# Performance work log

Measured on AMD Instinct MI355X. Metric: run time of the kernel, lower is better.

The kernel has to match this reference:

```python
import jax, jax.numpy as jnp
import numpy as np

N_NODES = 50000
N_EDGES = 600000
NUM_RELS = 5
IN_CH = 768
HID = 128
OUT_CH = 128
REL_DIM = 200


def _segment_softmax(scores, seg, n):
    # numerically stable softmax over variable-size segments (destination nodes)
    m = jax.ops.segment_max(scores, seg, num_segments=n)
    e = jnp.exp(scores - m[seg])
    s = jax.ops.segment_sum(e, seg, num_segments=n)
    return e / s[seg]


def _hgn_conv(x, edge_index, edge_type, W, Wr, a, Wres, rel_tab, final):
    # x: [N, h_in]; W: [h, h_in]; Wr: [h, rel_dim]; a: [3h]; rel_tab: [R, rel_dim]
    src = edge_index[0]
    dst = edge_index[1]
    n = x.shape[0]
    h = W.shape[0]
    Wx = x @ W.T                      # [N, h] (shared by x_i, x_j, messages)
    rel = rel_tab[edge_type] @ Wr.T   # [E, h]
    aA, aB, aC = a[:h], a[h:2 * h], a[2 * h:]
    # a([Wx_i | Wx_j | Wr rel]) decomposed to avoid materializing the concat
    score = Wx[dst] @ aA + Wx[src] @ aB + rel @ aC   # [E]
    alpha = jax.nn.leaky_relu(score, 0.2)
    alpha = _segment_softmax(alpha, dst, n)
    agg = jax.ops.segment_sum(Wx[src] * alpha[:, None], dst, num_segments=n)
    out = jax.nn.elu(agg + x @ Wres.T)
    if final:
        out = out / jnp.maximum(jnp.linalg.norm(out, axis=1, keepdims=True), 1e-12)
    return out, alpha


def setup_inputs() -> dict:
    key = jax.random.key(0)
    ks = jax.random.split(key, 20)
    s = 0.02
    return {
        "x": jax.random.normal(ks[0], (N_NODES, IN_CH), jnp.float32),
        "edge_index": jax.random.randint(ks[1], (2, N_EDGES), 0, N_NODES, jnp.int64 if jax.config.jax_enable_x64 else jnp.int32),
        "edge_type": jax.random.randint(ks[2], (N_EDGES,), 0, NUM_RELS, jnp.int64 if jax.config.jax_enable_x64 else jnp.int32),
        "l1_W": jax.random.normal(ks[3], (HID, IN_CH), jnp.float32) * s,
        "l1_b": jnp.zeros((HID,), jnp.float32),
        "l2_W": jax.random.normal(ks[4], (OUT_CH, HID), jnp.float32) * s,
        "l2_b": jnp.zeros((OUT_CH,), jnp.float32),
        "W1": jax.random.normal(ks[5], (HID, HID), jnp.float32) * s,
        "Wr1": jax.random.normal(ks[6], (HID, REL_DIM), jnp.float32) * s,
        "a1": jax.random.normal(ks[7], (3 * HID,), jnp.float32) * s,
        "Wres1": jax.random.normal(ks[8], (HID, HID), jnp.float32) * s,
        "rel1": jax.random.normal(ks[9], (NUM_RELS, REL_DIM), jnp.float32),
        "W2": jax.random.normal(ks[10], (HID, HID), jnp.float32) * s,
        "Wr2": jax.random.normal(ks[11], (HID, REL_DIM), jnp.float32) * s,
        "a2": jax.random.normal(ks[12], (3 * HID,), jnp.float32) * s,
        "Wres2": jax.random.normal(ks[13], (HID, HID), jnp.float32) * s,
        "rel2": jax.random.normal(ks[14], (NUM_RELS, REL_DIM), jnp.float32),
    }


def reference(x, edge_index, edge_type, l1_W, l1_b, l2_W, l2_b,
              W1, Wr1, a1, Wres1, rel1, W2, Wr2, a2, Wres2, rel2):
    out = jax.nn.leaky_relu(x @ l1_W.T + l1_b, 0.01)
    # layer 1 (dropout is identity in eval mode)
    out, alpha = _hgn_conv(out, edge_index, edge_type, W1, Wr1, a1, Wres1, rel1, final=False)
    # layer 2: original code blends alpha into self.alpha but weights messages
    # with its own (unblended) softmax alpha, so pre_alpha does not affect output
    out, _ = _hgn_conv(out, edge_index, edge_type, W2, Wr2, a2, Wres2, rel2, final=True)
    out = jax.nn.leaky_relu(out @ l2_W.T + l2_b, 0.01)
    return out
```

## Files before the change

kernel.cpp:

```cpp
#include <hip/hip_runtime.h>

namespace {

typedef unsigned short ushort_t;
typedef unsigned int uint_t;
typedef __attribute__((ext_vector_type(8))) short bf16x8;
typedef __attribute__((ext_vector_type(4))) float f32x4;

constexpr int N   = 50000;
constexpr int E   = 600000;
constexpr int NR  = 5;
constexpr int KIN = 768;
constexpr int H   = 128;
constexpr int RD  = 200;

__device__ inline ushort_t f2b(float f){
  uint_t u = __builtin_bit_cast(uint_t, f);
  uint_t r = (u + 0x7FFFu + ((u >> 16) & 1u)) >> 16;
  return (ushort_t)r;
}
__device__ inline float b2f_lo(uint_t u){ return __builtin_bit_cast(float, u << 16); }
__device__ inline float b2f_hi(uint_t u){ return __builtin_bit_cast(float, u & 0xFFFF0000u); }
__device__ inline float b2f_us(ushort_t h){ return __builtin_bit_cast(float, ((uint_t)h) << 16); }

__global__ void prep_k(const float* __restrict__ l1W, const float* __restrict__ W1,
                       const float* __restrict__ R1, const float* __restrict__ W2,
                       const float* __restrict__ R2, const float* __restrict__ l2W,
                       ushort_t* __restrict__ wts, int* __restrict__ deg,
                       const float* __restrict__ rel1, const float* __restrict__ Wr1,
                       const float* __restrict__ a1, float* __restrict__ sC1,
                       const float* __restrict__ rel2, const float* __restrict__ Wr2,
                       const float* __restrict__ a2, float* __restrict__ sC2){
  constexpr int S0 = H * KIN;
  constexpr int S1 = H * H;
  int b = blockIdx.x, tid = threadIdx.x;
  if (b < 704){
    int i = b * 256 + tid;
    float v;
    if (i < S0) v = l1W[i];
    else {
      int j = i - S0, seg = j >> 14, off = j & (S1 - 1);
      const float* srcs[5] = {W1, R1, W2, R2, l2W};
      v = srcs[seg][off];
    }
    wts[i] = f2b(v);
  } else if (b < 900){
    int i = (b - 704) * 256 + tid;
    if (i < N) deg[i] = 0;
  } else {
    int L = b - 900;
    const float* rel = L ? rel2 : rel1;
    const float* Wr  = L ? Wr2  : Wr1;
    const float* a   = L ? a2   : a1;
    float*       sC  = L ? sC2  : sC1;
    __shared__ float red[256];
    int n = tid >> 1, half = tid & 1;
    float aC = a[256 + n];
    for (int r = 0; r < NR; ++r){
      float p = 0.f;
      for (int k = half * 100; k < half * 100 + 100; ++k)
        p += rel[r * RD + k] * Wr[n * RD + k];
      red[tid] = p * aC;
      __syncthreads();
      for (int s = 128; s > 0; s >>= 1){
        if (tid < s) red[tid] += red[tid + s];
        __syncthreads();
      }
      if (tid == 0) sC[r] = red[0];
      __syncthreads();
    }
  }
}

__global__ void degcount_k(const int* __restrict__ dst, int* __restrict__ deg){
  int e = blockIdx.x * 256 + threadIdx.x;
  if (e < E) atomicAdd(&deg[dst[e]], 1);
}

__global__ void scan1_k(const int* __restrict__ deg, int* __restrict__ chunk,
                        int* __restrict__ bsums, int n){
  __shared__ int s[256];
  int tid = threadIdx.x, i = blockIdx.x * 256 + tid;
  int v = (i < n) ? deg[i] : 0;
  s[tid] = v; __syncthreads();
  for (int off = 1; off < 256; off <<= 1){
    int t = (tid >= off) ? s[tid - off] : 0;
    __syncthreads();
    s[tid] += t;
    __syncthreads();
  }
  if (i < n) chunk[i] = s[tid] - v;
  if (tid == 255) bsums[blockIdx.x] = s[255];
}

__global__ void scan2_k(const int* __restrict__ bsums, int* __restrict__ boffs, int nb){
  __shared__ int s[256];
  int tid = threadIdx.x;
  int v = (tid < nb) ? bsums[tid] : 0;
  s[tid] = v; __syncthreads();
  for (int off = 1; off < 256; off <<= 1){
    int t = (tid >= off) ? s[tid - off] : 0;
    __syncthreads();
    s[tid] += t;
    __syncthreads();
  }
  if (tid < nb) boffs[tid] = s[tid] - v;
}

__global__ void scan3_k(int* __restrict__ rowptr, const int* __restrict__ boffs,
                        int* __restrict__ cursor, int n, int total){
  int i = blockIdx.x * 256 + threadIdx.x;
  if (i < n){
    int v = rowptr[i] + boffs[blockIdx.x];
    rowptr[i] = v; cursor[i] = v;
  }
  if (i == 0) rowptr[n] = total;
}

__global__ void fill_k(const int* __restrict__ src, const int* __restrict__ dst,
                       const int* __restrict__ et, int* __restrict__ cursor,
                       int* __restrict__ cpk){
  int e = blockIdx.x * 256 + threadIdx.x;
  if (e < E){
    int d = dst[e];
    int p = atomicAdd(&cursor[d], 1);
    cpk[p] = src[e] | (et[e] << 16);
  }
}

template<int K1, int M1, bool AFP32, bool NORM, bool STORE1, int M2>
__global__ __launch_bounds__(256) void gfused_k(
    const void* __restrict__ Ap, const ushort_t* __restrict__ Wb1,
    const float* __restrict__ bias1, const ushort_t* __restrict__ aggM,
    ushort_t* __restrict__ out1,
    const ushort_t* __restrict__ Wb2, const float* __restrict__ vec2,
    void* __restrict__ out2, float* __restrict__ sA, float* __restrict__ sB, int M)
{
  constexpr int AP = 40;
  constexpr int BP = 40;
  constexpr int CP = 136;
  __shared__ __align__(16) ushort_t As[64 * AP];
  __shared__ __align__(16) ushort_t Bs[128 * BP];
  __shared__ __align__(16) ushort_t Cs[64 * CP];
  const int tid  = threadIdx.x;
  const int wave = tid >> 6, lane = tid & 63;
  const int l15  = lane & 15, quad = lane >> 4;
  const int row0 = blockIdx.x * 64;

  if (M1 == 2){
    #pragma unroll
    for (int i = 0; i < 4; ++i){
      int idx = tid + 256 * i;
      int r = idx >> 4, c8 = idx & 15;
      int grow = row0 + r;
      uint4 v = make_uint4(0, 0, 0, 0);
      if (grow < M) v = *reinterpret_cast<const uint4*>(aggM + (size_t)grow * 128 + c8 * 8);
      *reinterpret_cast<uint4*>(&Cs[r * CP + c8 * 8]) = v;
    }
  }

  f32x4 acc[8];
  #pragma unroll
  for (int t = 0; t < 8; ++t) acc[t] = (f32x4){0.f, 0.f, 0.f, 0.f};

  for (int k0 = 0; k0 < K1; k0 += 32){
    {
      int r = tid >> 2, q = tid & 3;
      int grow = row0 + r;
      ushort_t v[8] = {0,0,0,0,0,0,0,0};
      if (grow < M){
        if (AFP32){
          const float* ap = (const float*)Ap + (size_t)grow * K1 + k0 + q * 8;
          float4 u0 = *reinterpret_cast<const float4*>(ap);
          float4 u1 = *reinterpret_cast<const float4*>(ap + 4);
          v[0]=f2b(u0.x); v[1]=f2b(u0.y); v[2]=f2b(u0.z); v[3]=f2b(u0.w);
          v[4]=f2b(u1.x); v[5]=f2b(u1.y); v[6]=f2b(u1.z); v[7]=f2b(u1.w);
        } else {
          const uint4 u = *reinterpret_cast<const uint4*>(
              (const ushort_t*)Ap + (size_t)grow * K1 + k0 + q * 8);
          *reinterpret_cast<uint4*>(v) = u;
        }
      }
      *reinterpret_cast<uint4*>(&As[r * AP + q * 8]) = *reinterpret_cast<uint4*>(v);
    }
    {
      int n = tid >> 1, seg = tid & 1;
      const ushort_t* wp = Wb1 + (size_t)n * K1 + k0 + seg * 16;
      uint4 v0 = *reinterpret_cast<const uint4*>(wp);
      uint4 v1 = *reinterpret_cast<const uint4*>(wp + 8);
      *reinterpret_cast<uint4*>(&Bs[n * BP + seg * 16])     = v0;
      *reinterpret_cast<uint4*>(&Bs[n * BP + seg * 16 + 8]) = v1;
    }
    __syncthreads();
    bf16x8 af = *reinterpret_cast<const bf16x8*>(&As[(wave * 16 + l15) * AP + quad * 8]);
    #pragma unroll
    for (int t = 0; t < 8; ++t){
      bf16x8 bfr = *reinterpret_cast<const bf16x8*>(&Bs[(t * 16 + l15) * BP + quad * 8]);
      acc[t] = __builtin_amdgcn_mfma_f32_16x16x32_bf16(af, bfr, acc[t], 0, 0, 0);
    }
    __syncthreads();
  }

  float vv[8][4];
  #pragma unroll
  for (int t = 0; t < 8; ++t){
    #pragma unroll
    for (int r = 0; r < 4; ++r){
      int lr  = wave * 16 + quad * 4 + r;
      int col = t * 16 + l15;
      float v = acc[t][r];
      if (M1 == 1){
        v += bias1[col];
        v = v > 0.f ? v : 0.01f * v;
      } else {
        v += b2f_us(Cs[lr * CP + col]);
        v = v > 0.f ? v : __expf(v) - 1.f;
      }
      vv[t][r] = v;
    }
  }
  if (NORM){
    #pragma unroll
    for (int r = 0; r < 4; ++r){
      float ss = 0.f;
      #pragma unroll
      for (int t = 0; t < 8; ++t) ss += vv[t][r] * vv[t][r];
      #pragma unroll
      for (int off = 1; off < 16; off <<= 1) ss += __shfl_xor(ss, off, 64);
      float sc = 1.f / fmaxf(sqrtf(ss), 1e-12f);
      #pragma unroll
      for (int t = 0; t < 8; ++t) vv[t][r] *= sc;
    }
  }
  #pragma unroll
  for (int t = 0; t < 8; ++t){
    #pragma unroll
    for (int r = 0; r < 4; ++r){
      int lr  = wave * 16 + quad * 4 + r;
      int col = t * 16 + l15;
      int grow = row0 + lr;
      ushort_t h = f2b(vv[t][r]);
      if (STORE1 && grow < M) out1[(size_t)grow * 128 + col] = h;
      Cs[lr * CP + col] = h;
    }
  }
  __syncthreads();

  #pragma unroll
  for (int t = 0; t < 8; ++t) acc[t] = (f32x4){0.f, 0.f, 0.f, 0.f};
  for (int k0 = 0; k0 < 128; k0 += 32){
    {
      int n = tid >> 1, seg = tid & 1;
      const ushort_t* wp = Wb2 + (size_t)n * 128 + k0 + seg * 16;
      uint4 v0 = *reinterpret_cast<const uint4*>(wp);
      uint4 v1 = *reinterpret_cast<const uint4*>(wp + 8);
      *reinterpret_cast<uint4*>(&Bs[n * BP + seg * 16])     = v0;
      *reinterpret_cast<uint4*>(&Bs[n * BP + seg * 16 + 8]) = v1;
    }
    __syncthreads();
    bf16x8 af = *reinterpret_cast<const bf16x8*>(&Cs[(wave * 16 + l15) * CP + k0 + quad * 8]);
    #pragma unroll
    for (int t = 0; t < 8; ++t){
      bf16x8 bfr = *reinterpret_cast<const bf16x8*>(&Bs[(t * 16 + l15) * BP + quad * 8]);
      acc[t] = __builtin_amdgcn_mfma_f32_16x16x32_bf16(af, bfr, acc[t], 0, 0, 0);
    }
    __syncthreads();
  }

  if (M2 == 1){
    #pragma unroll
    for (int t = 0; t < 8; ++t){
      #pragma unroll
      for (int r = 0; r < 4; ++r){
        int grow = row0 + wave * 16 + quad * 4 + r;
        if (grow >= M) continue;
        int col = t * 16 + l15;
        float v = acc[t][r] + vec2[col];
        v = v > 0.f ? v : 0.01f * v;
        ((float*)out2)[(size_t)grow * 128 + col] = v;
      }
    }
  } else {
    #pragma unroll
    for (int t = 0; t < 8; ++t){
      #pragma unroll
      for (int r = 0; r < 4; ++r){
        int grow = row0 + wave * 16 + quad * 4 + r;
        if (grow >= M) continue;
        int col = t * 16 + l15;
        ((ushort_t*)out2)[(size_t)grow * 128 + col] = f2b(acc[t][r]);
      }
    }
    #pragma unroll
    for (int r = 0; r < 4; ++r){
      float pa = 0.f, pb = 0.f;
      #pragma unroll
      for (int t = 0; t < 8; ++t){
        int col = t * 16 + l15;
        pa += acc[t][r] * vec2[col];
        pb += acc[t][r] * vec2[128 + col];
      }
      #pragma unroll
      for (int off = 1; off < 16; off <<= 1){
        pa += __shfl_xor(pa, off, 64);
        pb += __shfl_xor(pb, off, 64);
      }
      int grow = row0 + wave * 16 + quad * 4 + r;
      if (l15 == r && grow < M){ sA[grow] = pa; sB[grow] = pb; }
    }
  }
}

__global__ void agg_k(const ushort_t* __restrict__ Wx, const float* __restrict__ sA,
                      const float* __restrict__ sB, const float* __restrict__ sC,
                      const int* __restrict__ rowptr, const int* __restrict__ cpk,
                      uint_t* __restrict__ aggU, int n){
  int node = blockIdx.x * 4 + (threadIdx.x >> 6);
  int lane = threadIdx.x & 63;
  if (node >= n) return;
  int p0 = rowptr[node], p1 = rowptr[node + 1];
  int deg = p1 - p0;
  float sa = sA[node];
  float m = -1e30f, ssum = 0.f, a0 = 0.f, a1 = 0.f;

  for (int c0 = 0; c0 < deg; c0 += 64){
    int cnt = deg - c0; if (cnt > 64) cnt = 64;
    bool ok = lane < cnt;
    int p  = p0 + c0 + (ok ? lane : 0);
    int pk = cpk[p];
    int sn = pk & 0xFFFF;
    float s = sa + sB[sn] + sC[pk >> 16];
    s = s > 0.f ? s : 0.2f * s;
    float sv = ok ? s : -1e30f;
    #pragma unroll
    for (int off = 32; off > 0; off >>= 1) sv = fmaxf(sv, __shfl_xor(sv, off, 64));
    float mn = fmaxf(m, sv);
    float corr = __expf(m - mn);
    ssum *= corr; a0 *= corr; a1 *= corr;
    float ev = ok ? __expf(s - mn) : 0.f;
    float es = ev;
    #pragma unroll
    for (int off = 32; off > 0; off >>= 1) es += __shfl_xor(es, off, 64);
    ssum += es;
    int png = ok ? pk : 0;
    m = mn;

    for (int e = 0; e < cnt; e += 4){
      int  n0 = __shfl(png, e,     64) & 0xFFFF, n1 = __shfl(png, e + 1, 64) & 0xFFFF;
      int  n2 = __shfl(png, e + 2, 64) & 0xFFFF, n3 = __shfl(png, e + 3, 64) & 0xFFFF;
      float e0 = __shfl(ev, e,     64), e1 = __shfl(ev, e + 1, 64);
      float e2 = __shfl(ev, e + 2, 64), e3 = __shfl(ev, e + 3, 64);
      uint_t u0 = *reinterpret_cast<const uint_t*>(Wx + (size_t)n0 * 128 + lane * 2);
      uint_t u1 = *reinterpret_cast<const uint_t*>(Wx + (size_t)n1 * 128 + lane * 2);
      uint_t u2 = *reinterpret_cast<const uint_t*>(Wx + (size_t)n2 * 128 + lane * 2);
      uint_t u3 = *reinterpret_cast<const uint_t*>(Wx + (size_t)n3 * 128 + lane * 2);
      a0 += e0 * b2f_lo(u0); a1 += e0 * b2f_hi(u0);
      a0 += e1 * b2f_lo(u1); a1 += e1 * b2f_hi(u1);
      a0 += e2 * b2f_lo(u2); a1 += e2 * b2f_hi(u2);
      a0 += e3 * b2f_lo(u3); a1 += e3 * b2f_hi(u3);
    }
  }
  float inv = (deg > 0) ? 1.f / ssum : 0.f;
  uint_t o = (uint_t)f2b(a0 * inv) | ((uint_t)f2b(a1 * inv) << 16);
  aggU[(size_t)node * 64 + lane] = o;
}

}

extern "C" void kernel_launch(void* const* d_in, const int* in_sizes, int n_in,
                              void* d_out, int out_size, void* d_ws, size_t ws_size,
                              hipStream_t stream)
{
  const float* x     = (const float*)d_in[0];
  const int*   eidx  = (const int*)d_in[1];
  const int*   et    = (const int*)d_in[2];
  const float* l1W   = (const float*)d_in[3];
  const float* l1b   = (const float*)d_in[4];
  const float* l2W   = (const float*)d_in[5];
  const float* l2b   = (const float*)d_in[6];
  const float* W1    = (const float*)d_in[7];
  const float* Wr1   = (const float*)d_in[8];
  const float* a1    = (const float*)d_in[9];
  const float* Wres1 = (const float*)d_in[10];
  const float* rel1  = (const float*)d_in[11];
  const float* W2    = (const float*)d_in[12];
  const float* Wr2   = (const float*)d_in[13];
  const float* a2    = (const float*)d_in[14];
  const float* Wres2 = (const float*)d_in[15];
  const float* rel2  = (const float*)d_in[16];
  float* outp = (float*)d_out;

  const int* esrc = eidx;
  const int* edst = eidx + E;

  float* f = (float*)d_ws;
  size_t o = 0;
  float* sA   = f + o; o += N;
  float* sB   = f + o; o += N;
  float* sC1  = f + o; o += 8;
  float* sC2  = f + o; o += 8;
  ushort_t* us = (ushort_t*)(f + o);
  size_t ou = 0;
  ushort_t* b0   = us + ou; ou += (size_t)N * H;
  ushort_t* b1   = us + ou; ou += (size_t)N * H;
  ushort_t* Wxb  = us + ou; ou += (size_t)N * H;
  ushort_t* aggB = us + ou; ou += (size_t)N * H;
  ushort_t* wtsb = us + ou; ou += (size_t)H * KIN + 5 * H * H;
  ushort_t* l1Wb = wtsb;
  ushort_t* W1b  = wtsb + H * KIN;
  ushort_t* R1b  = W1b + H * H;
  ushort_t* W2b  = R1b + H * H;
  ushort_t* R2b  = W2b + H * H;
  ushort_t* l2Wb = R2b + H * H;
  if (ou & 1) ou += 1;
  int* wi = (int*)(us + ou);
  size_t oi = 0;
  int* deg    = wi + oi; oi += N;
  int* rowptr = wi + oi; oi += N + 1;
  int* cursor = wi + oi; oi += N;
  int* bsums  = wi + oi; oi += 256;
  int* boffs  = wi + oi; oi += 256;
  int* cpk    = wi + oi; oi += E;

  const int EB    = (E + 255) / 256;
  const int NB256 = (N + 255) / 256;
  const int GB    = (N + 63) / 64;
  const int NB4   = (N + 3) / 4;

  prep_k<<<902, 256, 0, stream>>>(l1W, W1, Wres1, W2, Wres2, l2W, wtsb, deg,
                                  rel1, Wr1, a1, sC1, rel2, Wr2, a2, sC2);
  degcount_k<<<EB, 256, 0, stream>>>(edst, deg);
  scan1_k<<<NB256, 256, 0, stream>>>(deg, rowptr, bsums, N);
  scan2_k<<<1, 256, 0, stream>>>(bsums, boffs, NB256);
  scan3_k<<<NB256, 256, 0, stream>>>(rowptr, boffs, cursor, N, E);
  fill_k<<<EB, 256, 0, stream>>>(esrc, edst, et, cursor, cpk);

  gfused_k<KIN, 1, true, false, true, 3><<<GB, 256, 0, stream>>>(
      x, l1Wb, l1b, nullptr, b0, W1b, a1, Wxb, sA, sB, N);
  agg_k<<<NB4, 256, 0, stream>>>(Wxb, sA, sB, sC1, rowptr, cpk, (uint_t*)aggB, N);

  gfused_k<H, 2, false, false, true, 3><<<GB, 256, 0, stream>>>(
      b0, R1b, nullptr, aggB, b1, W2b, a2, Wxb, sA, sB, N);
  agg_k<<<NB4, 256, 0, stream>>>(Wxb, sA, sB, sC2, rowptr, cpk, (uint_t*)aggB, N);

  gfused_k<H, 2, false, true, false, 1><<<GB, 256, 0, stream>>>(
      b1, R2b, nullptr, aggB, nullptr, l2Wb, l2b, outp, nullptr, nullptr, N);
}
```

Baseline: 480.9 us.

## Merge all stages into one persistent cooperative kernel with grid syncs

Replaces the eleven separate kernel launches with one cooperative persistent kernel. Phases are separated by grid.sync, degree counting overlaps with the first GEMM through an atomic tile counter, and the aggregation uses grid-stride loops with an 8-way unrolled gather. The aim is to remove launch gaps and tail effects between the many small stages. In exchange it adds grid-wide barriers, caps the grid at 768 blocks under launch_bounds(256,2), and keeps the old multi-kernel path as a fallback if the cooperative launch fails.

New measurement: 554.9 us. 1.15x slower.

```diff
diff --git a/kernel.cpp b/kernel.cpp
--- a/kernel.cpp
+++ b/kernel.cpp
@@ -1,4 +1,7 @@
 #include <hip/hip_runtime.h>
+#include <hip/hip_cooperative_groups.h>
+
+namespace cg = cooperative_groups;
 
 namespace {
 
@@ -14,6 +17,10 @@
 constexpr int H   = 128;
 constexpr int RD  = 200;
 
+constexpr int NT     = 256;
+constexpr int NSCAN  = 196;
+constexpr int GTILES = (N + 63) / 64;
+
 __device__ inline ushort_t f2b(float f){
   uint_t u = __builtin_bit_cast(uint_t, f);
   uint_t r = (u + 0x7FFFu + ((u >> 16) & 1u)) >> 16;
@@ -23,129 +30,32 @@
 __device__ inline float b2f_hi(uint_t u){ return __builtin_bit_cast(float, u & 0xFFFF0000u); }
 __device__ inline float b2f_us(ushort_t h){ return __builtin_bit_cast(float, ((uint_t)h) << 16); }
 
-__global__ void prep_k(const float* __restrict__ l1W, const float* __restrict__ W1,
-                       const float* __restrict__ R1, const float* __restrict__ W2,
-                       const float* __restrict__ R2, const float* __restrict__ l2W,
-                       ushort_t* __restrict__ wts, int* __restrict__ deg,
-                       const float* __restrict__ rel1, const float* __restrict__ Wr1,
-                       const float* __restrict__ a1, float* __restrict__ sC1,
-                       const float* __restrict__ rel2, const float* __restrict__ Wr2,
-                       const float* __restrict__ a2, float* __restrict__ sC2){
-  constexpr int S0 = H * KIN;
-  constexpr int S1 = H * H;
-  int b = blockIdx.x, tid = threadIdx.x;
-  if (b < 704){
-    int i = b * 256 + tid;
-    float v;
-    if (i < S0) v = l1W[i];
-    else {
-      int j = i - S0, seg = j >> 14, off = j & (S1 - 1);
-      const float* srcs[5] = {W1, R1, W2, R2, l2W};
-      v = srcs[seg][off];
-    }
-    wts[i] = f2b(v);
-  } else if (b < 900){
-    int i = (b - 704) * 256 + tid;
-    if (i < N) deg[i] = 0;
-  } else {
-    int L = b - 900;
-    const float* rel = L ? rel2 : rel1;
-    const float* Wr  = L ? Wr2  : Wr1;
-    const float* a   = L ? a2   : a1;
-    float*       sC  = L ? sC2  : sC1;
-    __shared__ float red[256];
-    int n = tid >> 1, half = tid & 1;
-    float aC = a[256 + n];
-    for (int r = 0; r < NR; ++r){
-      float p = 0.f;
-      for (int k = half * 100; k < half * 100 + 100; ++k)
-        p += rel[r * RD + k] * Wr[n * RD + k];
-      red[tid] = p * aC;
-      __syncthreads();
-      for (int s = 128; s > 0; s >>= 1){
-        if (tid < s) red[tid] += red[tid + s];
-        __syncthreads();
-      }
-      if (tid == 0) sC[r] = red[0];
-      __syncthreads();
-    }
-  }
-}
-
-__global__ void degcount_k(const int* __restrict__ dst, int* __restrict__ deg){
-  int e = blockIdx.x * 256 + threadIdx.x;
-  if (e < E) atomicAdd(&deg[dst[e]], 1);
-}
-
-__global__ void scan1_k(const int* __restrict__ deg, int* __restrict__ chunk,
-                        int* __restrict__ bsums, int n){
-  __shared__ int s[256];
-  int tid = threadIdx.x, i = blockIdx.x * 256 + tid;
-  int v = (i < n) ? deg[i] : 0;
-  s[tid] = v; __syncthreads();
-  for (int off = 1; off < 256; off <<= 1){
-    int t = (tid >= off) ? s[tid - off] : 0;
-    __syncthreads();
-    s[tid] += t;
-    __syncthreads();
-  }
-  if (i < n) chunk[i] = s[tid] - v;
-  if (tid == 255) bsums[blockIdx.x] = s[255];
-}
-
-__global__ void scan2_k(const int* __restrict__ bsums, int* __restrict__ boffs, int nb){
-  __shared__ int s[256];
-  int tid = threadIdx.x;
-  int v = (tid < nb) ? bsums[tid] : 0;
-  s[tid] = v; __syncthreads();
-  for (int off = 1; off < 256; off <<= 1){
-    int t = (tid >= off) ? s[tid - off] : 0;
-    __syncthreads();
-    s[tid] += t;
-    __syncthreads();
-  }
-  if (tid < nb) boffs[tid] = s[tid] - v;
-}
-
-__global__ void scan3_k(int* __restrict__ rowptr, const int* __restrict__ boffs,
-                        int* __restrict__ cursor, int n, int total){
-  int i = blockIdx.x * 256 + threadIdx.x;
-  if (i < n){
-    int v = rowptr[i] + boffs[blockIdx.x];
-    rowptr[i] = v; cursor[i] = v;
-  }
-  if (i == 0) rowptr[n] = total;
-}
-
-__global__ void fill_k(const int* __restrict__ src, const int* __restrict__ dst,
-                       const int* __restrict__ et, int* __restrict__ cursor,
-                       int* __restrict__ cpk){
-  int e = blockIdx.x * 256 + threadIdx.x;
-  if (e < E){
-    int d = dst[e];
-    int p = atomicAdd(&cursor[d], 1);
-    cpk[p] = src[e] | (et[e] << 16);
-  }
-}
+struct Par {
+  const float* x; const int* esrc; const int* edst; const int* et;
+  const float* l1W; const float* l1b; const float* l2W; const float* l2b;
+  const float* W1;  const float* Wr1; const float* a1; const float* Wres1; const float* rel1;
+  const float* W2;  const float* Wr2; const float* a2; const float* Wres2; const float* rel2;
+  float* outp;
+  float* sA; float* sB; float* sC1; float* sC2;
+  ushort_t* b0; ushort_t* b1; ushort_t* Wxb; ushort_t* aggB;
+  ushort_t* l1Wb; ushort_t* W1b; ushort_t* R1b; ushort_t* W2b; ushort_t* R2b; ushort_t* l2Wb;
+  int* deg; int* rowptr; int* cursor; int* bsums; int* boffs; int* cpk; int* tileCtr;
+};
 
 template<int K1, int M1, bool AFP32, bool NORM, bool STORE1, int M2>
-__global__ __launch_bounds__(256) void gfused_k(
-    const void* __restrict__ Ap, const ushort_t* __restrict__ Wb1,
-    const float* __restrict__ bias1, const ushort_t* __restrict__ aggM,
-    ushort_t* __restrict__ out1,
-    const ushort_t* __restrict__ Wb2, const float* __restrict__ vec2,
-    void* __restrict__ out2, float* __restrict__ sA, float* __restrict__ sB, int M)
+__device__ void gtile(int row0, const void* Ap, const ushort_t* Wb1,
+                      const float* bias1, const ushort_t* aggM, ushort_t* out1,
+                      const ushort_t* Wb2, const float* vec2, void* out2,
+                      float* sA, float* sB, char* smem)
 {
-  constexpr int AP = 40;
-  constexpr int BP = 40;
-  constexpr int CP = 136;
-  __shared__ __align__(16) ushort_t As[64 * AP];
-  __shared__ __align__(16) ushort_t Bs[128 * BP];
-  __shared__ __align__(16) ushort_t Cs[64 * CP];
+  constexpr int AP = 40, BP = 40, CP = 136;
+  ushort_t* As = (ushort_t*)smem;
+  ushort_t* Bs = As + 64 * AP;
+  ushort_t* Cs = Bs + 128 * BP;
   const int tid  = threadIdx.x;
   const int wave = tid >> 6, lane = tid & 63;
   const int l15  = lane & 15, quad = lane >> 4;
-  const int row0 = blockIdx.x * 64;
+  const int M = N;
 
   if (M1 == 2){
     #pragma unroll
@@ -164,8 +74,7 @@
   for (int t = 0; t < 8; ++t) acc[t] = (f32x4){0.f, 0.f, 0.f, 0.f};
 
   for (int k0 = 0; k0 < K1; k0 += 32){
-    {
-      int r = tid >> 2, q = tid & 3;
+    { int r = tid >> 2, q = tid & 3;
       int grow = row0 + r;
       ushort_t v[8] = {0,0,0,0,0,0,0,0};
       if (grow < M){
@@ -183,8 +92,7 @@
       }
       *reinterpret_cast<uint4*>(&As[r * AP + q * 8]) = *reinterpret_cast<uint4*>(v);
     }
-    {
-      int n = tid >> 1, seg = tid & 1;
+    { int n = tid >> 1, seg = tid & 1;
       const ushort_t* wp = Wb1 + (size_t)n * K1 + k0 + seg * 16;
       uint4 v0 = *reinterpret_cast<const uint4*>(wp);
       uint4 v1 = *reinterpret_cast<const uint4*>(wp + 8);
@@ -249,8 +157,7 @@
   #pragma unroll
   for (int t = 0; t < 8; ++t) acc[t] = (f32x4){0.f, 0.f, 0.f, 0.f};
   for (int k0 = 0; k0 < 128; k0 += 32){
-    {
-      int n = tid >> 1, seg = tid & 1;
+    { int n = tid >> 1, seg = tid & 1;
       const ushort_t* wp = Wb2 + (size_t)n * 128 + k0 + seg * 16;
       uint4 v0 = *reinterpret_cast<const uint4*>(wp);
       uint4 v1 = *reinterpret_cast<const uint4*>(wp + 8);
@@ -309,60 +216,289 @@
       if (l15 == r && grow < M){ sA[grow] = pa; sB[grow] = pb; }
     }
   }
-}
-
-__global__ void agg_k(const ushort_t* __restrict__ Wx, const float* __restrict__ sA,
-                      const float* __restrict__ sB, const float* __restrict__ sC,
-                      const int* __restrict__ rowptr, const int* __restrict__ cpk,
-                      uint_t* __restrict__ aggU, int n){
-  int node = blockIdx.x * 4 + (threadIdx.x >> 6);
+  __syncthreads();
+}
+
+__device__ void agg_phase(const ushort_t* __restrict__ Wx, const float* __restrict__ sA,
+                          const float* __restrict__ sB, const float* __restrict__ sC,
+                          const int* __restrict__ rowptr, const int* __restrict__ cpk,
+                          uint_t* __restrict__ aggU)
+{
   int lane = threadIdx.x & 63;
-  if (node >= n) return;
-  int p0 = rowptr[node], p1 = rowptr[node + 1];
-  int deg = p1 - p0;
-  float sa = sA[node];
-  float m = -1e30f, ssum = 0.f, a0 = 0.f, a1 = 0.f;
-
-  for (int c0 = 0; c0 < deg; c0 += 64){
-    int cnt = deg - c0; if (cnt > 64) cnt = 64;
-    bool ok = lane < cnt;
-    int p  = p0 + c0 + (ok ? lane : 0);
-    int pk = cpk[p];
-    int sn = pk & 0xFFFF;
-    float s = sa + sB[sn] + sC[pk >> 16];
-    s = s > 0.f ? s : 0.2f * s;
-    float sv = ok ? s : -1e30f;
-    #pragma unroll
-    for (int off = 32; off > 0; off >>= 1) sv = fmaxf(sv, __shfl_xor(sv, off, 64));
-    float mn = fmaxf(m, sv);
-    float corr = __expf(m - mn);
-    ssum *= corr; a0 *= corr; a1 *= corr;
-    float ev = ok ? __expf(s - mn) : 0.f;
-    float es = ev;
-    #pragma unroll
-    for (int off = 32; off > 0; off >>= 1) es += __shfl_xor(es, off, 64);
-    ssum += es;
-    int png = ok ? pk : 0;
-    m = mn;
-
-    for (int e = 0; e < cnt; e += 4){
-      int  n0 = __shfl(png, e,     64) & 0xFFFF, n1 = __shfl(png, e + 1, 64) & 0xFFFF;
-      int  n2 = __shfl(png, e + 2, 64) & 0xFFFF, n3 = __shfl(png, e + 3, 64) & 0xFFFF;
-      float e0 = __shfl(ev, e,     64), e1 = __shfl(ev, e + 1, 64);
-      float e2 = __shfl(ev, e + 2, 64), e3 = __shfl(ev, e + 3, 64);
-      uint_t u0 = *reinterpret_cast<const uint_t*>(Wx + (size_t)n0 * 128 + lane * 2);
-      uint_t u1 = *reinterpret_cast<const uint_t*>(Wx + (size_t)n1 * 128 + lane * 2);
-      uint_t u2 = *reinterpret_cast<const uint_t*>(Wx + (size_t)n2 * 128 + lane * 2);
-      uint_t u3 = *reinterpret_cast<const uint_t*>(Wx + (size_t)n3 * 128 + lane * 2);
-      a0 += e0 * b2f_lo(u0); a1 += e0 * b2f_hi(u0);
-      a0 += e1 * b2f_lo(u1); a1 += e1 * b2f_hi(u1);
-      a0 += e2 * b2f_lo(u2); a1 += e2 * b2f_hi(u2);
-      a0 += e3 * b2f_lo(u3); a1 += e3 * b2f_hi(u3);
-    }
-  }
-  float inv = (deg > 0) ? 1.f / ssum : 0.f;
-  uint_t o = (uint_t)f2b(a0 * inv) | ((uint_t)f2b(a1 * inv) << 16);
-  aggU[(size_t)node * 64 + lane] = o;
+  int wid  = blockIdx.x * 4 + (threadIdx.x >> 6);
+  int wstride = gridDim.x * 4;
+  for (int node = wid; node < N; node += wstride){
+    int p0 = rowptr[node], p1 = rowptr[node + 1];
+    int deg = p1 - p0;
+    float sa = sA[node];
+    float m = -1e30f, ssum = 0.f, a0 = 0.f, a1 = 0.f;
+    for (int c0 = 0; c0 < deg; c0 += 64){
+      int cnt = deg - c0; if (cnt > 64) cnt = 64;
+      bool ok = lane < cnt;
+      int p  = p0 + c0 + (ok ? lane : 0);
+      int pk = cpk[p];
+      int sn = pk & 0xFFFF;
+      float s = sa + sB[sn] + sC[pk >> 16];
+      s = s > 0.f ? s : 0.2f * s;
+      float sv = ok ? s : -1e30f;
+      #pragma unroll
+      for (int off = 32; off > 0; off >>= 1) sv = fmaxf(sv, __shfl_xor(sv, off, 64));
+      float mn = fmaxf(m, sv);
+      float corr = __expf(m - mn);
+      ssum *= corr; a0 *= corr; a1 *= corr;
+      float ev = ok ? __expf(s - mn) : 0.f;
+      float es = ev;
+      #pragma unroll
+      for (int off = 32; off > 0; off >>= 1) es += __shfl_xor(es, off, 64);
+      ssum += es;
+      int png = ok ? pk : 0;
+      m = mn;
+      for (int e = 0; e < cnt; e += 8){
+        #pragma unroll
+        for (int j = 0; j < 8; ++j){
+          int  nj = __shfl(png, e + j, 64) & 0xFFFF;
+          float ej = __shfl(ev,  e + j, 64);
+          uint_t u = *reinterpret_cast<const uint_t*>(Wx + (size_t)nj * 128 + lane * 2);
+          a0 += ej * b2f_lo(u); a1 += ej * b2f_hi(u);
+        }
+      }
+    }
+    float inv = (deg > 0) ? 1.f / ssum : 0.f;
+    uint_t o = (uint_t)f2b(a0 * inv) | ((uint_t)f2b(a1 * inv) << 16);
+    aggU[(size_t)node * 64 + lane] = o;
+  }
+}
+
+__global__ __launch_bounds__(256, 2) void mega_k(Par p)
+{
+  cg::grid_group grid = cg::this_grid();
+  __shared__ __align__(16) char smem[32768];
+  __shared__ int tS;
+  const int b = blockIdx.x, tid = threadIdx.x;
+  const int G = gridDim.x;
+
+  {
+    constexpr int S0 = H * KIN, S1 = H * H, TOT = S0 + 5 * S1;
+    for (int i = b * NT + tid; i < TOT; i += G * NT){
+      float v;
+      if (i < S0) v = p.l1W[i];
+      else {
+        int j = i - S0, seg = j >> 14, off = j & (S1 - 1);
+        const float* srcs[5] = {p.W1, p.Wres1, p.W2, p.Wres2, p.l2W};
+        v = srcs[seg][off];
+      }
+      p.l1Wb[i] = f2b(v);
+    }
+    for (int i = b * NT + tid; i < N; i += G * NT) p.deg[i] = 0;
+    if (b == 0 && tid == 0) *p.tileCtr = 0;
+    if (b >= G - 2){
+      int L = b - (G - 2);
+      const float* rel = L ? p.rel2 : p.rel1;
+      const float* Wr  = L ? p.Wr2  : p.Wr1;
+      const float* a   = L ? p.a2   : p.a1;
+      float*       sC  = L ? p.sC2  : p.sC1;
+      float* red = (float*)smem;
+      int nn = tid >> 1, half = tid & 1;
+      float aC = a[256 + nn];
+      for (int r = 0; r < NR; ++r){
+        float acc = 0.f;
+        for (int k = half * 100; k < half * 100 + 100; ++k)
+          acc += rel[r * RD + k] * Wr[nn * RD + k];
+        red[tid] = acc * aC;
+        __syncthreads();
+        for (int s = 128; s > 0; s >>= 1){
+          if (tid < s) red[tid] += red[tid + s];
+          __syncthreads();
+        }
+        if (tid == 0) sC[r] = red[0];
+        __syncthreads();
+      }
+    }
+  }
+  __threadfence(); grid.sync();
+
+  if (b < NSCAN){
+    for (int e = b * NT + tid; e < E; e += NSCAN * NT) atomicAdd(&p.deg[p.edst[e]], 1);
+  }
+  while (true){
+    if (tid == 0) tS = atomicAdd(p.tileCtr, 1);
+    __syncthreads();
+    int t = tS;
+    if (t >= GTILES) break;
+    gtile<KIN, 1, true, false, true, 3>(t * 64, p.x, p.l1Wb, p.l1b, nullptr, p.b0,
+                                        p.W1b, p.a1, p.Wxb, p.sA, p.sB, smem);
+  }
+  __threadfence(); grid.sync();
+
+  if (b < NSCAN){
+    int* s = (int*)smem;
+    int i = b * 256 + tid;
+    int v = (i < N) ? p.deg[i] : 0;
+    s[tid] = v; __syncthreads();
+    for (int off = 1; off < 256; off <<= 1){
+      int t2 = (tid >= off) ? s[tid - off] : 0;
+      __syncthreads();
+      s[tid] += t2;
+      __syncthreads();
+    }
+    if (i < N) p.rowptr[i] = s[tid] - v;
+    if (tid == 255) p.bsums[b] = s[255];
+  }
+  __threadfence(); grid.sync();
+
+  if (b < NSCAN){
+    int* s = (int*)smem;
+    int v = (tid < NSCAN) ? p.bsums[tid] : 0;
+    s[tid] = v; __syncthreads();
+    for (int off = 1; off < 256; off <<= 1){
+      int t2 = (tid >= off) ? s[tid - off] : 0;
+      __syncthreads();
+      s[tid] += t2;
+      __syncthreads();
+    }
+    int boff = (b == 0) ? 0 : s[b - 1];
+    int i = b * 256 + tid;
+    if (i < N){
+      int r = p.rowptr[i] + boff;
+      p.rowptr[i] = r; p.cursor[i] = r;
+    }
+    if (b == 0 && tid == 0) p.rowptr[N] = E;
+  }
+  __threadfence(); grid.sync();
+
+  for (int e = b * NT + tid; e < E; e += G * NT){
+    int d = p.edst[e];
+    int pos = atomicAdd(&p.cursor[d], 1);
+    p.cpk[pos] = p.esrc[e] | (p.et[e] << 16);
+  }
+  __threadfence(); grid.sync();
+
+  agg_phase(p.Wxb, p.sA, p.sB, p.sC1, p.rowptr, p.cpk, (uint_t*)p.aggB);
+  __threadfence(); grid.sync();
+
+  for (int t = b; t < GTILES; t += G)
+    gtile<H, 2, false, false, true, 3>(t * 64, p.b0, p.R1b, nullptr, p.aggB, p.b1,
+                                       p.W2b, p.a2, p.Wxb, p.sA, p.sB, smem);
+  __threadfence(); grid.sync();
+
+  agg_phase(p.Wxb, p.sA, p.sB, p.sC2, p.rowptr, p.cpk, (uint_t*)p.aggB);
+  __threadfence(); grid.sync();
+
+  for (int t = b; t < GTILES; t += G)
+    gtile<H, 2, false, true, false, 1>(t * 64, p.b1, p.R2b, nullptr, p.aggB, nullptr,
+                                       p.l2Wb, p.l2b, p.outp, nullptr, nullptr, smem);
+}
+
+__global__ void prep_k(Par p){
+  constexpr int S0 = H * KIN, S1 = H * H;
+  int b = blockIdx.x, tid = threadIdx.x;
+  if (b < 704){
+    int i = b * 256 + tid;
+    float v;
+    if (i < S0) v = p.l1W[i];
+    else {
+      int j = i - S0, seg = j >> 14, off = j & (S1 - 1);
+      const float* srcs[5] = {p.W1, p.Wres1, p.W2, p.Wres2, p.l2W};
+      v = srcs[seg][off];
+    }
+    p.l1Wb[i] = f2b(v);
+  } else if (b < 900){
+    int i = (b - 704) * 256 + tid;
+    if (i < N) p.deg[i] = 0;
+  } else {
+    int L = b - 900;
+    const float* rel = L ? p.rel2 : p.rel1;
+    const float* Wr  = L ? p.Wr2  : p.Wr1;
+    const float* a   = L ? p.a2   : p.a1;
+    float*       sC  = L ? p.sC2  : p.sC1;
+    __shared__ float red[256];
+    int nn = tid >> 1, half = tid & 1;
+    float aC = a[256 + nn];
+    for (int r = 0; r < NR; ++r){
+      float acc = 0.f;
+      for (int k = half * 100; k < half * 100 + 100; ++k)
+        acc += rel[r * RD + k] * Wr[nn * RD + k];
+      red[tid] = acc * aC;
+      __syncthreads();
+      for (int s = 128; s > 0; s >>= 1){
+        if (tid < s) red[tid] += red[tid + s];
+        __syncthreads();
+      }
+      if (tid == 0) sC[r] = red[0];
+      __syncthreads();
+    }
+  }
+}
+
+__global__ void degcount_k(const int* __restrict__ dst, int* __restrict__ deg){
+  int e = blockIdx.x * 256 + threadIdx.x;
+  if (e < E) atomicAdd(&deg[dst[e]], 1);
+}
+
+__global__ void scan1_k(const int* __restrict__ deg, int* __restrict__ chunk,
+                        int* __restrict__ bsums, int n){
+  __shared__ int s[256];
+  int tid = threadIdx.x, i = blockIdx.x * 256 + tid;
+  int v = (i < n) ? deg[i] : 0;
+  s[tid] = v; __syncthreads();
+  for (int off = 1; off < 256; off <<= 1){
+    int t = (tid >= off) ? s[tid - off] : 0;
+    __syncthreads();
+    s[tid] += t;
+    __syncthreads();
+  }
+  if (i < n) chunk[i] = s[tid] - v;
+  if (tid == 255) bsums[blockIdx.x] = s[255];
+}
+
+__global__ void scan2_k(const int* __restrict__ bsums, int* __restrict__ boffs, int nb){
+  __shared__ int s[256];
+  int tid = threadIdx.x;
+  int v = (tid < nb) ? bsums[tid] : 0;
+  s[tid] = v; __syncthreads();
+  for (int off = 1; off < 256; off <<= 1){
+    int t = (tid >= off) ? s[tid - off] : 0;
+    __syncthreads();
+    s[tid] += t;
+    __syncthreads();
+  }
+  if (tid < nb) boffs[tid] = s[tid] - v;
+}
+
+__global__ void scan3_k(int* __restrict__ rowptr, const int* __restrict__ boffs,
+                        int* __restrict__ cursor, int n, int total){
+  int i = blockIdx.x * 256 + threadIdx.x;
+  if (i < n){
+    int v = rowptr[i] + boffs[blockIdx.x];
+    rowptr[i] = v; cursor[i] = v;
+  }
+  if (i == 0) rowptr[n] = total;
+}
+
+__global__ void fill_k(const int* __restrict__ src, const int* __restrict__ dst,
+                       const int* __restrict__ et, int* __restrict__ cursor,
+                       int* __restrict__ cpk){
+  int e = blockIdx.x * 256 + threadIdx.x;
+  if (e < E){
+    int d = dst[e];
+    int pp = atomicAdd(&cursor[d], 1);
+    cpk[pp] = src[e] | (et[e] << 16);
+  }
+}
+
+template<int K1, int M1, bool AFP32, bool NORM, bool STORE1, int M2>
+__global__ __launch_bounds__(256) void gfused_k(
+    const void* Ap, const ushort_t* Wb1, const float* bias1, const ushort_t* aggM,
+    ushort_t* out1, const ushort_t* Wb2, const float* vec2, void* out2,
+    float* sA, float* sB){
+  __shared__ __align__(16) char smem[32768];
+  gtile<K1, M1, AFP32, NORM, STORE1, M2>(blockIdx.x * 64, Ap, Wb1, bias1, aggM, out1,
+                                         Wb2, vec2, out2, sA, sB, smem);
+}
+
+__global__ void agg_k(const ushort_t* Wx, const float* sA, const float* sB,
+                      const float* sC, const int* rowptr, const int* cpk, uint_t* aggU){
+  agg_phase(Wx, sA, sB, sC, rowptr, cpk, aggU);
 }
 
 }
@@ -371,78 +507,91 @@
                               void* d_out, int out_size, void* d_ws, size_t ws_size,
                               hipStream_t stream)
 {
-  const float* x     = (const float*)d_in[0];
-  const int*   eidx  = (const int*)d_in[1];
-  const int*   et    = (const int*)d_in[2];
-  const float* l1W   = (const float*)d_in[3];
-  const float* l1b   = (const float*)d_in[4];
-  const float* l2W   = (const float*)d_in[5];
-  const float* l2b   = (const float*)d_in[6];
-  const float* W1    = (const float*)d_in[7];
-  const float* Wr1   = (const float*)d_in[8];
-  const float* a1    = (const float*)d_in[9];
-  const float* Wres1 = (const float*)d_in[10];
-  const float* rel1  = (const float*)d_in[11];
-  const float* W2    = (const float*)d_in[12];
-  const float* Wr2   = (const float*)d_in[13];
-  const float* a2    = (const float*)d_in[14];
-  const float* Wres2 = (const float*)d_in[15];
-  const float* rel2  = (const float*)d_in[16];
-  float* outp = (float*)d_out;
-
-  const int* esrc = eidx;
-  const int* edst = eidx + E;
+  Par p;
+  p.x     = (const float*)d_in[0];
+  const int* eidx = (const int*)d_in[1];
+  p.esrc  = eidx;
+  p.edst  = eidx + E;
+  p.et    = (const int*)d_in[2];
+  p.l1W   = (const float*)d_in[3];
+  p.l1b   = (const float*)d_in[4];
+  p.l2W   = (const float*)d_in[5];
+  p.l2b   = (const float*)d_in[6];
+  p.W1    = (const float*)d_in[7];
+  p.Wr1   = (const float*)d_in[8];
+  p.a1    = (const float*)d_in[9];
+  p.Wres1 = (const float*)d_in[10];
+  p.rel1  = (const float*)d_in[11];
+  p.W2    = (const float*)d_in[12];
+  p.Wr2   = (const float*)d_in[13];
+  p.a2    = (const float*)d_in[14];
+  p.Wres2 = (const float*)d_in[15];
+  p.rel2  = (const float*)d_in[16];
+  p.outp  = (float*)d_out;
 
   float* f = (float*)d_ws;
   size_t o = 0;
-  float* sA   = f + o; o += N;
-  float* sB   = f + o; o += N;
-  float* sC1  = f + o; o += 8;
-  float* sC2  = f + o; o += 8;
+  p.sA  = f + o; o += N;
+  p.sB  = f + o; o += N;
+  p.sC1 = f + o; o += 8;
+  p.sC2 = f + o; o += 8;
   ushort_t* us = (ushort_t*)(f + o);
   size_t ou = 0;
-  ushort_t* b0   = us + ou; ou += (size_t)N * H;
-  ushort_t* b1   = us + ou; ou += (size_t)N * H;
-  ushort_t* Wxb  = us + ou; ou += (size_t)N * H;
-  ushort_t* aggB = us + ou; ou += (size_t)N * H;
-  ushort_t* wtsb = us + ou; ou += (size_t)H * KIN + 5 * H * H;
-  ushort_t* l1Wb = wtsb;
-  ushort_t* W1b  = wtsb + H * KIN;
-  ushort_t* R1b  = W1b + H * H;
-  ushort_t* W2b  = R1b + H * H;
-  ushort_t* R2b  = W2b + H * H;
-  ushort_t* l2Wb = R2b + H * H;
-  if (ou & 1) ou += 1;
+  p.b0   = us + ou; ou += (size_t)N * H;
+  p.b1   = us + ou; ou += (size_t)N * H;
+  p.Wxb  = us + ou; ou += (size_t)N * H;
+  p.aggB = us + ou; ou += (size_t)N * H;
+  p.l1Wb = us + ou; ou += (size_t)H * KIN + 5 * H * H;
+  p.W1b  = p.l1Wb + H * KIN;
+  p.R1b  = p.W1b + H * H;
+  p.W2b  = p.R1b + H * H;
+  p.R2b  = p.W2b + H * H;
+  p.l2Wb = p.R2b + H * H;
+  ou = (ou + 1) & ~(size_t)1;
   int* wi = (int*)(us + ou);
   size_t oi = 0;
-  int* deg    = wi + oi; oi += N;
-  int* rowptr = wi + oi; oi += N + 1;
-  int* cursor = wi + oi; oi += N;
-  int* bsums  = wi + oi; oi += 256;
-  int* boffs  = wi + oi; oi += 256;
-  int* cpk    = wi + oi; oi += E;
-
-  const int EB    = (E + 255) / 256;
-  const int NB256 = (N + 255) / 256;
-  const int GB    = (N + 63) / 64;
-  const int NB4   = (N + 3) / 4;
-
-  prep_k<<<902, 256, 0, stream>>>(l1W, W1, Wres1, W2, Wres2, l2W, wtsb, deg,
-                                  rel1, Wr1, a1, sC1, rel2, Wr2, a2, sC2);
-  degcount_k<<<EB, 256, 0, stream>>>(edst, deg);
-  scan1_k<<<NB256, 256, 0, stream>>>(deg, rowptr, bsums, N);
-  scan2_k<<<1, 256, 0, stream>>>(bsums, boffs, NB256);
-  scan3_k<<<NB256, 256, 0, stream>>>(rowptr, boffs, cursor, N, E);
-  fill_k<<<EB, 256, 0, stream>>>(esrc, edst, et, cursor, cpk);
-
-  gfused_k<KIN, 1, true, false, true, 3><<<GB, 256, 0, stream>>>(
-      x, l1Wb, l1b, nullptr, b0, W1b, a1, Wxb, sA, sB, N);
-  agg_k<<<NB4, 256, 0, stream>>>(Wxb, sA, sB, sC1, rowptr, cpk, (uint_t*)aggB, N);
-
-  gfused_k<H, 2, false, false, true, 3><<<GB, 256, 0, stream>>>(
-      b0, R1b, nullptr, aggB, b1, W2b, a2, Wxb, sA, sB, N);
-  agg_k<<<NB4, 256, 0, stream>>>(Wxb, sA, sB, sC2, rowptr, cpk, (uint_t*)aggB, N);
-
-  gfused_k<H, 2, false, true, false, 1><<<GB, 256, 0, stream>>>(
-      b1, R2b, nullptr, aggB, nullptr, l2Wb, l2b, outp, nullptr, nullptr, N);
-}
+  p.deg     = wi + oi; oi += N;
+  p.rowptr  = wi + oi; oi += N + 1;
+  p.cursor  = wi + oi; oi += N;
+  p.bsums   = wi + oi; oi += 256;
+  p.boffs   = wi + oi; oi += 256;
+  p.cpk     = wi + oi; oi += E;
+  p.tileCtr = wi + oi; oi += 4;
+
+  hipError_t err = hipErrorUnknown;
+  int dev = 0;
+  (void)hipGetDevice(&dev);
+  int numCU = 0, maxB = 0;
+  (void)hipDeviceGetAttribute(&numCU, hipDeviceAttributeMultiprocessorCount, dev);
+  hipError_t oe = hipOccupancyMaxActiveBlocksPerMultiprocessor(&maxB, mega_k, NT, 0);
+  int grid = (oe == hipSuccess && numCU > 0 && maxB > 0) ? maxB * numCU : 0;
+  if (grid > 768) grid = 768;
+  if (grid >= 208){
+    void* args[] = { &p };
+    err = hipLaunchCooperativeKernel((const void*)mega_k, dim3(grid), dim3(NT), args, 0, stream);
+  }
+
+  if (err != hipSuccess){
+    const int EB    = (E + 255) / 256;
+    const int NB256 = (N + 255) / 256;
+    const int GB    = GTILES;
+    const int NB4   = (N + 3) / 4;
+    prep_k<<<902, 256, 0, stream>>>(p);
+    degcount_k<<<EB, 256, 0, stream>>>(p.edst, p.deg);
+    scan1_k<<<NB256, 256, 0, stream>>>(p.deg, p.rowptr, p.bsums, N);
+    scan2_k<<<1, 256, 0, stream>>>(p.bsums, p.boffs, NB256);
+    scan3_k<<<NB256, 256, 0, stream>>>(p.rowptr, p.boffs, p.cursor, N, E);
+    fill_k<<<EB, 256, 0, stream>>>(p.esrc, p.edst, p.et, p.cursor, p.cpk);
+
+    gfused_k<KIN, 1, true, false, true, 3><<<GB, 256, 0, stream>>>(
+        p.x, p.l1Wb, p.l1b, nullptr, p.b0, p.W1b, p.a1, p.Wxb, p.sA, p.sB);
+    agg_k<<<NB4, 256, 0, stream>>>(p.Wxb, p.sA, p.sB, p.sC1, p.rowptr, p.cpk, (uint_t*)p.aggB);
+
+    gfused_k<H, 2, false, false, true, 3><<<GB, 256, 0, stream>>>(
+        p.b0, p.R1b, nullptr, p.aggB, p.b1, p.W2b, p.a2, p.Wxb, p.sA, p.sB);
+    agg_k<<<NB4, 256, 0, stream>>>(p.Wxb, p.sA, p.sB, p.sC2, p.rowptr, p.cpk, (uint_t*)p.aggB);
+
+    gfused_k<H, 2, false, true, false, 1><<<GB, 256, 0, stream>>>(
+        p.b1, p.R2b, nullptr, p.aggB, nullptr, p.l2Wb, p.l2b, p.outp, nullptr, nullptr);
+  }
+}
```
